# Performance work log

Hardware: AMD Instinct MI355X
Metric: run time of the kernel (lower is better)

The kernel has to match this reference:

```python
import jax, jax.numpy as jnp
import numpy as np

B, V, NX, R, D, H = 512, 2, 1024, 64, 512, 8
S, NC, HS = 4, 2, 64           # bc_state_dim, num_controls, state-branch hidden
FIN = S * HS + 128             # fusion input dim (state feats + control feats)


def _ln(x, g, b, eps=1e-5):
    mu = jnp.mean(x, axis=-1, keepdims=True)
    var = jnp.mean((x - mu) ** 2, axis=-1, keepdims=True)
    return (x - mu) * jax.lax.rsqrt(var + eps) * g + b


def setup_inputs() -> dict:
    key = jax.random.key(0)
    ks = iter(jax.random.split(key, 64))
    def rn(shape, s=0.02):
        return jax.random.normal(next(ks), shape, dtype=jnp.float32) * s
    inp = {}
    inp['a_n'] = jax.random.normal(next(ks), (B, V, R), dtype=jnp.float32)
    inp['BC_Ctrl'] = jax.random.normal(next(ks), (B, S + NC), dtype=jnp.float32)
    inp['Phi'] = rn((V, NX, R), 1.0 / np.sqrt(NX).astype(np.float32))
    # per-variable attention params (stacked on leading V axis)
    inp['Wq_w'] = rn((V, 1, D));   inp['Wq_b'] = rn((V, D))
    inp['Wk_w'] = rn((V, NX, D));  inp['Wk_b'] = rn((V, D))
    inp['Wv_w'] = rn((V, NX, D));  inp['Wv_b'] = rn((V, D))
    inp['attn_ow'] = rn((V, D, D)); inp['attn_ob'] = rn((V, D))
    inp['proj_w'] = rn((V, D, 1));  inp['proj_b'] = rn((V, 1))
    # ImprovedUpdateFFN (num_layers=3, hidden=d_model) + LayerNorm
    inp['ffn_w1'] = rn((V, R, D)); inp['ffn_b1'] = rn((V, D))
    inp['ffn_w2'] = rn((V, D, D)); inp['ffn_b2'] = rn((V, D))
    inp['ffn_w3'] = rn((V, D, R)); inp['ffn_b3'] = rn((V, R))
    inp['ffn_ln_g'] = jnp.ones((V, R), jnp.float32)
    inp['ffn_ln_b'] = jnp.zeros((V, R), jnp.float32)
    # a0_mapping: Linear -> ReLU -> LayerNorm
    inp['a0_w'] = rn((V, R, R)); inp['a0_b'] = rn((V, R))
    inp['a0_ln_g'] = jnp.ones((V, R), jnp.float32)
    inp['a0_ln_b'] = jnp.zeros((V, R), jnp.float32)
    inp['alpha'] = jnp.full((V,), 0.1, jnp.float32)
    # UniversalLifting params
    inp['sb_w'] = rn((S, 1, HS)); inp['sb_b'] = rn((S, HS))
    inp['cm_w1'] = rn((NC, 64));  inp['cm_b1'] = rn((64,))
    inp['cm_w2'] = rn((64, 128)); inp['cm_b2'] = rn((128,))
    inp['fu_w1'] = rn((FIN, 256)); inp['fu_b1'] = rn((256,))
    inp['fu_w2'] = rn((256, 512)); inp['fu_b2'] = rn((512,))
    inp['fu_w3'] = rn((512, 256)); inp['fu_b3'] = rn((256,))
    inp['fu_w4'] = rn((256, V * NX)); inp['fu_b4'] = rn((V * NX,))
    return inp


def reference(a_n, BC_Ctrl, Phi, Wq_w, Wq_b, Wk_w, Wk_b, Wv_w, Wv_b,
              attn_ow, attn_ob, proj_w, proj_b,
              ffn_w1, ffn_b1, ffn_w2, ffn_b2, ffn_w3, ffn_b3, ffn_ln_g, ffn_ln_b,
              a0_w, a0_b, a0_ln_g, a0_ln_b, alpha,
              sb_w, sb_b, cm_w1, cm_b1, cm_w2, cm_b2,
              fu_w1, fu_b1, fu_w2, fu_b2, fu_w3, fu_b3, fu_w4, fu_b4):
    gelu = jax.nn.gelu
    # ---- UniversalLifting: U_B [B, V, NX] ----
    bs = BC_Ctrl[:, :S]                                              # [B,S]
    sf = gelu(bs[:, :, None] * sb_w[None, :, 0, :] + sb_b[None])     # [B,S,HS]
    sf = sf.reshape(bs.shape[0], S * HS)
    cf = gelu(BC_Ctrl[:, S:] @ cm_w1 + cm_b1)
    cf = gelu(cf @ cm_w2 + cm_b2)
    f = jnp.concatenate([sf, cf], axis=-1)                           # [B,FIN]
    h = gelu(f @ fu_w1 + fu_b1)
    h = gelu(h @ fu_w2 + fu_b2)
    h = gelu(h @ fu_w3 + fu_b3)
    U_B = (h @ fu_w4 + fu_b4).reshape(-1, V, NX)
    # ---- a0 mapping: Linear -> ReLU -> LayerNorm ----
    a_map = jax.nn.relu(jnp.einsum('bvr,vrs->bvs', a_n, a0_w) + a0_b[None])
    a_map = _ln(a_map, a0_ln_g[None], a0_ln_b[None])                 # [B,V,R]
    # ---- ImprovedUpdateFFN residual update ----
    h1 = gelu(jnp.einsum('bvr,vrd->bvd', a_map, ffn_w1) + ffn_b1[None])
    h2 = gelu(jnp.einsum('bvd,vde->bve', h1, ffn_w2) + ffn_b2[None])
    o = jnp.einsum('bvd,vdr->bvr', h2, ffn_w3) + ffn_b3[None]
    ffn_update = _ln(o + a_map, ffn_ln_g[None], ffn_ln_b[None])      # [B,V,R]
    # ---- Q/K/V; K,V depend only on Phi (batch-independent) ----
    Q = a_map[:, :, :, None] * Wq_w[:, 0][None, :, None, :] + Wq_b[None, :, None, :]  # [B,V,R,D]
    K = jnp.einsum('vnr,vnd->vrd', Phi, Wk_w) + Wk_b[:, None, :]     # [V,R,D]
    Vm = jnp.einsum('vnr,vnd->vrd', Phi, Wv_w) + Wv_b[:, None, :]    # [V,R,D]
    hd = D // H
    Qh = Q.reshape(-1, V, R, H, hd)
    Kh = K.reshape(V, R, H, hd)
    Vh = Vm.reshape(V, R, H, hd)
    # softmax-free linear attention: z = Q (K^T V) per head
    KV = jnp.einsum('vrhk,vrhl->vhkl', Kh, Vh)                        # [V,H,hd,hd]
    z = jnp.einsum('bvrhk,vhkl->bvrhl', Qh, KV).reshape(-1, V, R, D)
    z = jnp.einsum('bvrd,vde->bvre', z, attn_ow) + attn_ob[None, :, None, :]
    z = z / jnp.sqrt(jnp.float32(D))
    a_update = jnp.einsum('bvrd,vdo->bvro', z, proj_w)[..., 0] + proj_b[:, 0][None, :, None]
    a_next = a_map + a_update + alpha[None, :, None] * ffn_update     # [B,V,R]
    U_hat = jnp.einsum('vnr,bvr->bvn', Phi, a_next) + U_B             # [B,V,NX]
    return U_hat
```

## Files before the change

### kernel.cpp

```cpp
#include <hip/hip_runtime.h>
#include <hip/hip_bf16.h>
#include <math.h>


typedef unsigned short ushort_t;
using short8 = __attribute__((ext_vector_type(8))) short;
using f32x4  = __attribute__((ext_vector_type(4))) float;

__device__ __forceinline__ float gelu_f(float x) {
    float x3 = x*x*x;
    return 0.5f*x*(1.0f + tanhf(0.7978845608028654f*(x + 0.044715f*x3)));
}

__device__ __forceinline__ float wave_sum(float x) {
    #pragma unroll
    for (int m = 32; m >= 1; m >>= 1) x += __shfl_xor(x, m, 64);
    return x;
}

__device__ __forceinline__ ushort_t f2bf(float x) {
    unsigned u = __float_as_uint(x);
    unsigned r = (u + 0x7FFFu + ((u >> 16) & 1u)) >> 16;
    return (ushort_t)r;
}
__device__ __forceinline__ float bf2f(ushort_t h) {
    return __uint_as_float(((unsigned)h) << 16);
}

struct Ptrs {
    const float *a_n, *BC, *Wq_w, *Wq_b, *Wk_b, *Wv_b, *attn_ow, *attn_ob,
                *proj_w, *proj_b, *ffn_w3, *ffn_b3, *ffn_ln_g, *ffn_ln_b,
                *a0_w, *a0_b, *a0_ln_g, *a0_ln_b, *alpha,
                *sb_w, *sb_b, *cm_w1, *cm_b1, *cm_w2, *cm_b2,
                *fu_b1, *fu_b2, *fu_b3, *fu_b4, *ffn_b1, *ffn_b2;
    float *Kws, *Vws, *KV, *parts, *UB, *out;
    ushort_t *amap_bf, *anext_bf, *h1_bf, *h2_bf, *fbuf_bf, *hA_bf, *hB_bf, *hC_bf;
    ushort_t *w_fu1t, *w_fu2t, *w_fu3t, *w_fu4t, *w_ffn1t, *w_ffn2t,
             *Phi_bf, *Wk_t, *Wv_t, *Phi_t;
};

struct CvtDesc { const float* src; ushort_t* dst; int K, N, flat; };
struct CvtArgs { CvtDesc d[15]; int cum[16]; };

__device__ void cvt_dev(char* smem, int tile, const CvtDesc& d)
{
    const int t = threadIdx.x;
    if (d.flat) {
        const long base = (long)tile*4096 + t*16;
        const float4* s = (const float4*)(d.src + base);
        ushort4* o = (ushort4*)(d.dst + base);
        #pragma unroll
        for (int i = 0; i < 4; ++i) {
            float4 v = s[i];
            ushort4 w; w.x=f2bf(v.x); w.y=f2bf(v.y); w.z=f2bf(v.z); w.w=f2bf(v.w);
            o[i] = w;
        }
    } else {
        float* tl = (float*)smem;
        const int ntn = d.N >> 5;
        const int kt = tile / ntn, nt = tile % ntn;
        const int r = t >> 3, c0 = (t & 7) * 4;
        float4 v = *(const float4*)(d.src + (long)(kt*32 + r)*d.N + nt*32 + c0);
        tl[r*33 + c0] = v.x; tl[r*33 + c0+1] = v.y;
        tl[r*33 + c0+2] = v.z; tl[r*33 + c0+3] = v.w;
        __syncthreads();
        ushort4 w;
        w.x = f2bf(tl[(c0+0)*33 + r]); w.y = f2bf(tl[(c0+1)*33 + r]);
        w.z = f2bf(tl[(c0+2)*33 + r]); w.w = f2bf(tl[(c0+3)*33 + r]);
        *(ushort4*)(d.dst + (long)(nt*32 + r)*d.K + kt*32 + c0) = w;
    }
}

__device__ void bgemm_dev(char* smem_,
    const ushort_t* __restrict__ A, const ushort_t* __restrict__ B,
    const float* __restrict__ bias, const float* __restrict__ Add,
    void* __restrict__ Cv, int m0, int n0, int K, int ldc, int ldadd,
    int EPI, bool OUTBF)
{
    ushort_t* lds = (ushort_t*)smem_;
    const int tid = threadIdx.x;
    const int w = tid >> 6, l = tid & 63;
    const int ml = l & 15, kg = l >> 4;
    const int srow = tid >> 2, sslot = tid & 3;
    const ushort_t* Ag = A + (long)(m0 + srow)*K + sslot*8;
    const ushort_t* Bg = B + (long)(n0 + srow)*K + sslot*8;
    auto L = [&](int buf, int ab, int row, int col) {
        return lds + (((buf*2 + ab)*64 + row)*40 + col);
    };
    f32x4 acc[4] = {};
    const int nt = K >> 5;
    int4 ra = *(const int4*)Ag;
    int4 rb = *(const int4*)Bg;
    *(int4*)L(0,0,srow,sslot*8) = ra;
    *(int4*)L(0,1,srow,sslot*8) = rb;
    __syncthreads();
    for (int t = 0; t < nt; ++t) {
        const int cur = t & 1;
        if (t + 1 < nt) {
            ra = *(const int4*)(Ag + (t+1)*32);
            rb = *(const int4*)(Bg + (t+1)*32);
        }
        short8 af = *(const short8*)L(cur,0,w*16 + ml,kg*8);
        #pragma unroll
        for (int f = 0; f < 4; ++f) {
            short8 bfr = *(const short8*)L(cur,1,f*16 + ml,kg*8);
            acc[f] = __builtin_amdgcn_mfma_f32_16x16x32_bf16(af, bfr, acc[f], 0, 0, 0);
        }
        if (t + 1 < nt) {
            *(int4*)L(cur^1,0,srow,sslot*8) = ra;
            *(int4*)L(cur^1,1,srow,sslot*8) = rb;
            __syncthreads();
        }
    }
    float* Cf = (float*)Cv; ushort_t* Cb = (ushort_t*)Cv;
    const int mr = m0 + w*16 + kg*4;
    const int nc = n0 + ml;
    #pragma unroll
    for (int f = 0; f < 4; ++f) {
        const int n = nc + f*16;
        const float bs = (EPI != 2) ? bias[n] : 0.0f;
        #pragma unroll
        for (int r = 0; r < 4; ++r) {
            float x = acc[f][r] + bs;
            if (EPI == 1) x = gelu_f(x);
            if (EPI == 2) x = acc[f][r] + Add[(long)(mr + r)*ldadd + n];
            if (OUTBF) Cb[(long)(mr + r)*ldc + n] = f2bf(x);
            else       Cf[(long)(mr + r)*ldc + n] = x;
        }
    }
}

__device__ void control_dev(char* smem, int b, const Ptrs& p)
{
    float* bc  = (float*)smem;
    float* cf1 = bc + 8;
    const int tid = threadIdx.x;
    if (tid < 6) bc[tid] = p.BC[b*6 + tid];
    __syncthreads();
    {
        int s = tid >> 6;
        p.fbuf_bf[(long)b*384 + tid] = f2bf(gelu_f(bc[s]*p.sb_w[tid] + p.sb_b[tid]));
    }
    if (tid < 64) {
        cf1[tid] = gelu_f(bc[4]*p.cm_w1[tid] + bc[5]*p.cm_w1[64+tid] + p.cm_b1[tid]);
    }
    __syncthreads();
    if (tid < 128) {
        float acc = p.cm_b2[tid];
        #pragma unroll 8
        for (int i = 0; i < 64; ++i) acc = fmaf(cf1[i], p.cm_w2[i*128 + tid], acc);
        p.fbuf_bf[(long)b*384 + 256 + tid] = f2bf(gelu_f(acc));
    }
}

__device__ void a_map_dev(char* smem, int bx, int v, const Ptrs& p)
{
    float* arow = (float*)smem;
    const int w = threadIdx.x >> 6, lane = threadIdx.x & 63;
    const int b = bx*4 + w;
    arow[w*64 + lane] = p.a_n[((long)b*2 + v)*64 + lane];
    __syncthreads();
    float acc = p.a0_b[v*64 + lane];
    #pragma unroll 8
    for (int rp = 0; rp < 64; ++rp)
        acc = fmaf(arow[w*64 + rp], p.a0_w[((long)v*64 + rp)*64 + lane], acc);
    float x = fmaxf(acc, 0.0f);
    float mu = wave_sum(x) * (1.0f/64.0f);
    float d = x - mu;
    float var = wave_sum(d*d) * (1.0f/64.0f);
    float y = d * rsqrtf(var + 1e-5f) * p.a0_ln_g[v*64 + lane] + p.a0_ln_b[v*64 + lane];
    p.amap_bf[((long)v*512 + b)*64 + lane] = f2bf(y);
}

__device__ void kv_outer_dev(char* smem, int z, const Ptrs& p)
{
    const int v = z >> 3, h = z & 7;
    float* Ks = (float*)smem;
    float* Vs = Ks + 4096;
    const int tid = threadIdx.x;
    for (int idx = tid; idx < 4096; idx += 256) {
        int r = idx >> 6, c = idx & 63;
        long off = ((long)v*64 + r)*512 + h*64 + c;
        Ks[idx] = p.Kws[off];
        Vs[idx] = p.Vws[off];
    }
    __syncthreads();
    const int tx = tid & 15, ty = tid >> 4;
    float acc[4][4] = {};
    #pragma unroll 4
    for (int r = 0; r < 64; ++r) {
        float a[4], bb[4];
        #pragma unroll
        for (int i = 0; i < 4; ++i) a[i] = Ks[r*64 + ty*4+i];
        #pragma unroll
        for (int j = 0; j < 4; ++j) bb[j] = Vs[r*64 + tx*4+j];
        #pragma unroll
        for (int i = 0; i < 4; ++i)
            #pragma unroll
            for (int j = 0; j < 4; ++j)
                acc[i][j] = fmaf(a[i], bb[j], acc[i][j]);
    }
    #pragma unroll
    for (int i = 0; i < 4; ++i)
        #pragma unroll
        for (int j = 0; j < 4; ++j)
            p.KV[(((long)v*8 + h)*64 + ty*4+i)*64 + tx*4+j] = acc[i][j];
}

__device__ void attn_parts_dev(char* smem, int v, int ec, const Ptrs& p)
{
    float* Pv  = (float*)smem;
    float* Qv  = Pv + 512;
    float* red = Qv + 512;
    const int tid = threadIdx.x;
    for (int dp = tid; dp < 512; dp += 256) {
        int h = dp >> 6, l = dp & 63;
        const float* kvp = p.KV + ((long)(v*8 + h)*64)*64 + l;
        const float* wq = p.Wq_w + v*512 + h*64;
        const float* wb = p.Wq_b + v*512 + h*64;
        float pp = 0.f, q = 0.f;
        #pragma unroll 8
        for (int k = 0; k < 64; ++k) {
            float kv = kvp[(long)k*64];
            pp = fmaf(wq[k], kv, pp);
            q  = fmaf(wb[k], kv, q);
        }
        Pv[dp] = pp; Qv[dp] = q;
    }
    __syncthreads();
    const int e = ec*64 + (tid & 63);
    const int qd = tid >> 6;
    float pw = 0.f, qw = 0.f;
    const float* owp = p.attn_ow + (long)v*512*512 + e;
    #pragma unroll 8
    for (int d = qd*128; d < qd*128 + 128; ++d) {
        float wv = owp[(long)d*512];
        pw = fmaf(Pv[d], wv, pw);
        qw = fmaf(Qv[d], wv, qw);
    }
    red[tid] = pw; red[256 + tid] = qw;
    __syncthreads();
    if (tid < 64) {
        float PW = red[tid] + red[tid+64] + red[tid+128] + red[tid+192];
        float QW = red[256+tid] + red[256+tid+64] + red[256+tid+128] + red[256+tid+192];
        QW += p.attn_ob[v*512 + ec*64 + tid];
        float pj = p.proj_w[v*512 + ec*64 + tid];
        float pc1 = wave_sum(PW*pj);
        float pc0 = wave_sum(QW*pj);
        if (tid == 0) {
            p.parts[v*8 + ec]      = pc1;
            p.parts[16 + v*8 + ec] = pc0;
        }
    }
}

__device__ void ofuse_dev(char* smem, int bx, int v, const Ptrs& p)
{
    float* hrow = (float*)smem;
    const int w = threadIdx.x >> 6, lane = threadIdx.x & 63;
    const int b = bx*4 + w;
    const ushort_t* h2p = p.h2_bf + ((long)v*512 + b)*512;
    #pragma unroll
    for (int i = 0; i < 8; ++i) hrow[w*512 + lane + i*64] = bf2f(h2p[lane + i*64]);
    __syncthreads();
    float acc = p.ffn_b3[v*64 + lane];
    const float* w3p = p.ffn_w3 + (long)v*512*64 + lane;
    #pragma unroll 8
    for (int d = 0; d < 512; ++d)
        acc = fmaf(hrow[w*512 + d], w3p[(long)d*64], acc);
    const float am = bf2f(p.amap_bf[((long)v*512 + b)*64 + lane]);
    float t = acc + am;
    float mu = wave_sum(t) * (1.0f/64.0f);
    float dd = t - mu;
    float var = wave_sum(dd*dd) * (1.0f/64.0f);
    float u = dd * rsqrtf(var + 1e-5f) * p.ffn_ln_g[v*64+lane] + p.ffn_ln_b[v*64+lane];
    float s1 = 0.f, s0 = 0.f;
    #pragma unroll
    for (int c = 0; c < 8; ++c) { s1 += p.parts[v*8 + c]; s0 += p.parts[16 + v*8 + c]; }
    const float inv = 0.044194173824159216f;
    const float c1 = s1*inv, c0 = s0*inv + p.proj_b[v];
    p.anext_bf[((long)v*512 + b)*64 + lane] = f2bf(am*(1.0f + c1) + c0 + p.alpha[v]*u);
}

__global__ __launch_bounds__(256) void stage0_k(Ptrs p, CvtArgs ca, int ncvt)
{
    extern __shared__ char smem[];
    const int bx = blockIdx.x;
    if (bx < ncvt) {
        int e = 0;
        while (bx >= ca.cum[e+1]) ++e;
        cvt_dev(smem, bx - ca.cum[e], ca.d[e]);
    } else if (bx < ncvt + 512) {
        control_dev(smem, bx - ncvt, p);
    } else {
        int i = bx - ncvt - 512;
        a_map_dev(smem, i & 127, i >> 7, p);
    }
}

__global__ __launch_bounds__(256) void stage1_k(Ptrs p)
{
    extern __shared__ char smem[];
    const int bx = blockIdx.x;
    if (bx < 32) {
        int by = bx >> 2, bxx = bx & 3;
        bgemm_dev(smem, p.fbuf_bf, p.w_fu1t, p.fu_b1, nullptr, p.hA_bf,
                  by*64, bxx*64, 384, 256, 0, 1, true);
    } else if (bx < 160) {
        int i = bx - 32; int v = i >> 6; i &= 63; int by = i >> 3, bxx = i & 7;
        bgemm_dev(smem, p.amap_bf + (long)v*32768, p.w_ffn1t + (long)v*32768,
                  p.ffn_b1 + v*512, nullptr, (void*)(p.h1_bf + (long)v*262144),
                  by*64, bxx*64, 64, 512, 0, 1, true);
    } else {
        int i = bx - 160; int which = i >> 4; int v = (i >> 3) & 1; int bxx = i & 7;
        const ushort_t* Wt = which ? p.Wv_t : p.Wk_t;
        const float* Wb = which ? p.Wv_b : p.Wk_b;
        float* C = which ? p.Vws : p.Kws;
        bgemm_dev(smem, p.Phi_t + (long)v*65536, Wt + (long)v*524288,
                  Wb + v*512, nullptr, (void*)(C + (long)v*32768),
                  0, bxx*64, 1024, 512, 0, 0, false);
    }
}

__global__ __launch_bounds__(256) void stage2_k(Ptrs p)
{
    extern __shared__ char smem[];
    const int bx = blockIdx.x;
    if (bx < 64) {
        int by = bx >> 3, bxx = bx & 7;
        bgemm_dev(smem, p.hA_bf, p.w_fu2t, p.fu_b2, nullptr, p.hB_bf,
                  by*64, bxx*64, 256, 512, 0, 1, true);
    } else if (bx < 192) {
        int i = bx - 64; int v = i >> 6; i &= 63; int by = i >> 3, bxx = i & 7;
        bgemm_dev(smem, p.h1_bf + (long)v*262144, p.w_ffn2t + (long)v*262144,
                  p.ffn_b2 + v*512, nullptr, (void*)(p.h2_bf + (long)v*262144),
                  by*64, bxx*64, 512, 512, 0, 1, true);
    } else {
        kv_outer_dev(smem, bx - 192, p);
    }
}

__global__ __launch_bounds__(256) void stage3_k(Ptrs p)
{
    extern __shared__ char smem[];
    const int bx = blockIdx.x;
    if (bx < 32) {
        int by = bx >> 2, bxx = bx & 3;
        bgemm_dev(smem, p.hB_bf, p.w_fu3t, p.fu_b3, nullptr, p.hC_bf,
                  by*64, bxx*64, 512, 256, 0, 1, true);
    } else {
        int i = bx - 32;
        attn_parts_dev(smem, i & 1, i >> 1, p);
    }
}

__global__ __launch_bounds__(256) void stage4_k(Ptrs p)
{
    extern __shared__ char smem[];
    const int bx = blockIdx.x;
    if (bx < 256) {
        int by = bx >> 5, bxx = bx & 31;
        bgemm_dev(smem, p.hC_bf, p.w_fu4t, p.fu_b4, nullptr, p.UB,
                  by*64, bxx*64, 256, 2048, 0, 0, false);
    } else {
        int i = bx - 256;
        ofuse_dev(smem, i & 127, i >> 7, p);
    }
}

__global__ __launch_bounds__(256) void stage5_k(Ptrs p)
{
    extern __shared__ char smem[];
    const int bx = blockIdx.x;
    int v = bx >> 7; int rem = bx & 127; int by = rem >> 4, bxx = rem & 15;
    bgemm_dev(smem, p.anext_bf + (long)v*32768, p.Phi_bf + (long)v*65536,
              nullptr, p.UB + v*1024, (void*)(p.out + v*1024),
              by*64, bxx*64, 64, 2048, 2048, 2, false);
}

extern "C" void kernel_launch(void* const* d_in, const int* in_sizes, int n_in,
                              void* d_out, int out_size, void* d_ws, size_t ws_size,
                              hipStream_t stream)
{
    const float* a_n      = (const float*)d_in[0];
    const float* BC       = (const float*)d_in[1];
    const float* Phi      = (const float*)d_in[2];
    const float* Wq_w     = (const float*)d_in[3];
    const float* Wq_b     = (const float*)d_in[4];
    const float* Wk_w     = (const float*)d_in[5];
    const float* Wk_b     = (const float*)d_in[6];
    const float* Wv_w     = (const float*)d_in[7];
    const float* Wv_b     = (const float*)d_in[8];
    const float* attn_ow  = (const float*)d_in[9];
    const float* attn_ob  = (const float*)d_in[10];
    const float* proj_w   = (const float*)d_in[11];
    const float* proj_b   = (const float*)d_in[12];
    const float* ffn_w1   = (const float*)d_in[13];
    const float* ffn_b1   = (const float*)d_in[14];
    const float* ffn_w2   = (const float*)d_in[15];
    const float* ffn_b2   = (const float*)d_in[16];
    const float* ffn_w3   = (const float*)d_in[17];
    const float* ffn_b3   = (const float*)d_in[18];
    const float* ffn_ln_g = (const float*)d_in[19];
    const float* ffn_ln_b = (const float*)d_in[20];
    const float* a0_w     = (const float*)d_in[21];
    const float* a0_b     = (const float*)d_in[22];
    const float* a0_ln_g  = (const float*)d_in[23];
    const float* a0_ln_b  = (const float*)d_in[24];
    const float* alpha    = (const float*)d_in[25];
    const float* sb_w     = (const float*)d_in[26];
    const float* sb_b     = (const float*)d_in[27];
    const float* cm_w1    = (const float*)d_in[28];
    const float* cm_b1    = (const float*)d_in[29];
    const float* cm_w2    = (const float*)d_in[30];
    const float* cm_b2    = (const float*)d_in[31];
    const float* fu_w1    = (const float*)d_in[32];
    const float* fu_b1    = (const float*)d_in[33];
    const float* fu_w2    = (const float*)d_in[34];
    const float* fu_b2    = (const float*)d_in[35];
    const float* fu_w3    = (const float*)d_in[36];
    const float* fu_b3    = (const float*)d_in[37];
    const float* fu_w4    = (const float*)d_in[38];
    const float* fu_b4    = (const float*)d_in[39];

    float* ws = (float*)d_ws;
    Ptrs p;
    p.a_n = a_n; p.BC = BC; p.Wq_w = Wq_w; p.Wq_b = Wq_b; p.Wk_b = Wk_b; p.Wv_b = Wv_b;
    p.attn_ow = attn_ow; p.attn_ob = attn_ob; p.proj_w = proj_w; p.proj_b = proj_b;
    p.ffn_w3 = ffn_w3; p.ffn_b3 = ffn_b3; p.ffn_ln_g = ffn_ln_g; p.ffn_ln_b = ffn_ln_b;
    p.a0_w = a0_w; p.a0_b = a0_b; p.a0_ln_g = a0_ln_g; p.a0_ln_b = a0_ln_b;
    p.alpha = alpha; p.sb_w = sb_w; p.sb_b = sb_b;
    p.cm_w1 = cm_w1; p.cm_b1 = cm_b1; p.cm_w2 = cm_w2; p.cm_b2 = cm_b2;
    p.fu_b1 = fu_b1; p.fu_b2 = fu_b2; p.fu_b3 = fu_b3; p.fu_b4 = fu_b4;
    p.ffn_b1 = ffn_b1; p.ffn_b2 = ffn_b2;

    p.Kws      = ws;
    p.Vws      = ws + 65536;
    p.KV       = ws + 131072;
    p.parts    = ws + 196608;
    p.amap_bf  = (ushort_t*)(ws + 196736);
    p.anext_bf = (ushort_t*)(ws + 229504);
    p.h1_bf    = (ushort_t*)(ws + 262272);
    p.h2_bf    = (ushort_t*)(ws + 524416);
    p.fbuf_bf  = (ushort_t*)(ws + 786560);
    p.hA_bf    = (ushort_t*)(ws + 884864);
    p.hB_bf    = (ushort_t*)(ws + 950400);
    p.hC_bf    = (ushort_t*)(ws + 1081472);
    p.w_fu1t   = (ushort_t*)(ws + 1147008);
    p.w_fu2t   = (ushort_t*)(ws + 1196160);
    p.w_fu3t   = (ushort_t*)(ws + 1261696);
    p.w_fu4t   = (ushort_t*)(ws + 1327232);
    p.w_ffn1t  = (ushort_t*)(ws + 1589376);
    p.w_ffn2t  = (ushort_t*)(ws + 1622144);
    p.Phi_bf   = (ushort_t*)(ws + 1884288);
    p.UB       = ws + 1949824;
    p.Wk_t     = (ushort_t*)p.UB;
    p.Wv_t     = ((ushort_t*)p.UB) + 1048576;
    p.Phi_t    = (ushort_t*)(ws + 2998400);
    p.out      = (float*)d_out;

    CvtArgs ca;
    auto set = [&](int i, const float* s, ushort_t* dst, int K, int N, int flat) {
        ca.d[i].src = s; ca.d[i].dst = dst; ca.d[i].K = K; ca.d[i].N = N; ca.d[i].flat = flat;
    };
    set(0,  fu_w1,           p.w_fu1t,           384, 256,  0);
    set(1,  fu_w2,           p.w_fu2t,           256, 512,  0);
    set(2,  fu_w3,           p.w_fu3t,           512, 256,  0);
    set(3,  fu_w4,           p.w_fu4t,           256, 2048, 0);
    set(4,  ffn_w1,          p.w_ffn1t,          64,  512,  0);
    set(5,  ffn_w1 + 32768,  p.w_ffn1t + 32768,  64,  512,  0);
    set(6,  ffn_w2,          p.w_ffn2t,          512, 512,  0);
    set(7,  ffn_w2 + 262144, p.w_ffn2t + 262144, 512, 512,  0);
    set(8,  Phi,             p.Phi_bf,           131072, 0, 1);
    set(9,  Phi,             p.Phi_t,            1024, 64,  0);
    set(10, Phi + 65536,     p.Phi_t + 65536,    1024, 64,  0);
    set(11, Wk_w,            p.Wk_t,             1024, 512, 0);
    set(12, Wk_w + 524288,   p.Wk_t + 524288,    1024, 512, 0);
    set(13, Wv_w,            p.Wv_t,             1024, 512, 0);
    set(14, Wv_w + 524288,   p.Wv_t + 524288,    1024, 512, 0);
    const int tl[15] = {96,128,128,512,32,32,256,256,32,64,64,512,512,512,512};
    ca.cum[0] = 0;
    for (int i = 0; i < 15; ++i) ca.cum[i+1] = ca.cum[i] + tl[i];
    const int ncvt = ca.cum[15];

    stage0_k<<<ncvt + 768, 256, 4352,  stream>>>(p, ca, ncvt);
    stage1_k<<<192,        256, 20480, stream>>>(p);
    stage2_k<<<208,        256, 32768, stream>>>(p);
    stage3_k<<<48,         256, 20480, stream>>>(p);
    stage4_k<<<512,        256, 20480, stream>>>(p);
    stage5_k<<<256,        256, 20480, stream>>>(p);
}
```

Baseline: 77.58 us.

## Fold attention into per-variable scalars and merge final GEMMs into one K=384 GEMM

The batch-independent K/V/out-projection chain is collapsed algebraically. Matrix-vector products (attn_ow·proj_w, Wk·Wq, Wv·opj, then contractions with Phi) reduce the whole attention branch to two scalars per variable. This removes the large Phi×Wk/Wv GEMMs, the KV outer products and their bf16 conversions. The fusion-net output GEMM and the Phi reconstruction GEMM are combined into a single GEMM over a concatenated K dimension, with a precomputed bias row, which cuts one launch and the UB round trip. The cost is a different summation order, so numerical results may shift slightly.

```diff
diff --git a/kernel.cpp b/kernel.cpp
--- a/kernel.cpp
+++ b/kernel.cpp
@@ -28,33 +28,41 @@
 }
 
 struct Ptrs {
-    const float *a_n, *BC, *Wq_w, *Wq_b, *Wk_b, *Wv_b, *attn_ow, *attn_ob,
-                *proj_w, *proj_b, *ffn_w3, *ffn_b3, *ffn_ln_g, *ffn_ln_b,
+    const float *a_n, *BC, *Phi, *Wq_w, *Wq_b, *Wk_w, *Wk_b, *Wv_w, *Wv_b,
+                *attn_ow, *attn_ob, *proj_w, *proj_b,
+                *ffn_w3, *ffn_b3, *ffn_ln_g, *ffn_ln_b,
                 *a0_w, *a0_b, *a0_ln_g, *a0_ln_b, *alpha,
                 *sb_w, *sb_b, *cm_w1, *cm_b1, *cm_w2, *cm_b2,
                 *fu_b1, *fu_b2, *fu_b3, *fu_b4, *ffn_b1, *ffn_b2;
-    float *Kws, *Vws, *KV, *parts, *UB, *out;
-    ushort_t *amap_bf, *anext_bf, *h1_bf, *h2_bf, *fbuf_bf, *hA_bf, *hB_bf, *hC_bf;
-    ushort_t *w_fu1t, *w_fu2t, *w_fu3t, *w_fu4t, *w_ffn1t, *w_ffn2t,
-             *Phi_bf, *Wk_t, *Wv_t, *Phi_t;
+    float *opj, *u0, *u1, *u2, *pkq, *pqq, *parts, *phirs, *bias2, *out;
+    ushort_t *amap_bf, *h1_bf, *h2_bf, *fbuf_bf, *hA_bf, *hB_bf;
+    ushort_t *w_fu1t, *w_fu2t, *w_fu3t, *w_ffn1t, *w_ffn2t, *Abig, *Bbig;
 };
 
-struct CvtDesc { const float* src; ushort_t* dst; int K, N, flat; };
-struct CvtArgs { CvtDesc d[15]; int cum[16]; };
-
-__device__ void cvt_dev(char* smem, int tile, const CvtDesc& d)
+struct CvtDesc { const float* src; ushort_t* dst; int K, N, mode, ldd, coff; };
+struct CvtArgs { CvtDesc d[10]; int cum[11]; };
+
+__device__ void cvt_dev(char* smem, int tile, const CvtDesc& d, const Ptrs& p)
 {
     const int t = threadIdx.x;
-    if (d.flat) {
-        const long base = (long)tile*4096 + t*16;
-        const float4* s = (const float4*)(d.src + base);
-        ushort4* o = (ushort4*)(d.dst + base);
+    if (d.mode == 2) {
+        const int row = t >> 2, q = t & 3;
+        const float* s = d.src + (long)(tile*64 + row)*64 + q*16;
+        ushort_t* dst  = d.dst + (long)(tile*64 + row)*384 + d.coff + q*16;
+        ushort_t* dz   = d.dst + (long)(tile*64 + row)*384 + (64 - d.coff) + q*16;
+        float sum = 0.f;
         #pragma unroll
         for (int i = 0; i < 4; ++i) {
-            float4 v = s[i];
-            ushort4 w; w.x=f2bf(v.x); w.y=f2bf(v.y); w.z=f2bf(v.z); w.w=f2bf(v.w);
-            o[i] = w;
-        }
+            float4 x = *(const float4*)(s + i*4);
+            ushort4 w; w.x=f2bf(x.x); w.y=f2bf(x.y); w.z=f2bf(x.z); w.w=f2bf(x.w);
+            *(ushort4*)(dst + i*4) = w;
+            ushort4 z; z.x=0; z.y=0; z.z=0; z.w=0;
+            *(ushort4*)(dz + i*4) = z;
+            sum += x.x + x.y + x.z + x.w;
+        }
+        sum += __shfl_xor(sum, 1, 64);
+        sum += __shfl_xor(sum, 2, 64);
+        if (q == 0) p.phirs[d.K + tile*64 + row] = sum;
     } else {
         float* tl = (float*)smem;
         const int ntn = d.N >> 5;
@@ -67,14 +75,14 @@
         ushort4 w;
         w.x = f2bf(tl[(c0+0)*33 + r]); w.y = f2bf(tl[(c0+1)*33 + r]);
         w.z = f2bf(tl[(c0+2)*33 + r]); w.w = f2bf(tl[(c0+3)*33 + r]);
-        *(ushort4*)(d.dst + (long)(nt*32 + r)*d.K + kt*32 + c0) = w;
+        *(ushort4*)(d.dst + (long)(nt*32 + r)*d.ldd + d.coff + kt*32 + c0) = w;
     }
 }
 
 __device__ void bgemm_dev(char* smem_,
     const ushort_t* __restrict__ A, const ushort_t* __restrict__ B,
-    const float* __restrict__ bias, const float* __restrict__ Add,
-    void* __restrict__ Cv, int m0, int n0, int K, int ldc, int ldadd,
+    const float* __restrict__ bias,
+    void* __restrict__ Cv, int m0, int n0, int K, int ldc,
     int EPI, bool OUTBF)
 {
     ushort_t* lds = (ushort_t*)smem_;
@@ -118,12 +126,11 @@
     #pragma unroll
     for (int f = 0; f < 4; ++f) {
         const int n = nc + f*16;
-        const float bs = (EPI != 2) ? bias[n] : 0.0f;
+        const float bs = bias[n];
         #pragma unroll
         for (int r = 0; r < 4; ++r) {
             float x = acc[f][r] + bs;
             if (EPI == 1) x = gelu_f(x);
-            if (EPI == 2) x = acc[f][r] + Add[(long)(mr + r)*ldadd + n];
             if (OUTBF) Cb[(long)(mr + r)*ldc + n] = f2bf(x);
             else       Cf[(long)(mr + r)*ldc + n] = x;
         }
@@ -172,85 +179,143 @@
     p.amap_bf[((long)v*512 + b)*64 + lane] = f2bf(y);
 }
 
-__device__ void kv_outer_dev(char* smem, int z, const Ptrs& p)
-{
-    const int v = z >> 3, h = z & 7;
-    float* Ks = (float*)smem;
-    float* Vs = Ks + 4096;
-    const int tid = threadIdx.x;
-    for (int idx = tid; idx < 4096; idx += 256) {
-        int r = idx >> 6, c = idx & 63;
-        long off = ((long)v*64 + r)*512 + h*64 + c;
-        Ks[idx] = p.Kws[off];
-        Vs[idx] = p.Vws[off];
-    }
+__device__ void opj_dev(int oi, const Ptrs& p)
+{
+    const int tid = threadIdx.x;
+    const int v = oi >> 3, dc = oi & 7;
+    const int d = dc*64 + (tid >> 2);
+    const int e0 = (tid & 3)*128;
+    const float* row = p.attn_ow + ((long)v*512 + d)*512 + e0;
+    const float* pj  = p.proj_w + v*512 + e0;
+    float s = 0.f;
+    #pragma unroll 8
+    for (int j = 0; j < 128; ++j) s = fmaf(row[j], pj[j], s);
+    s += __shfl_xor(s, 1, 64);
+    s += __shfl_xor(s, 2, 64);
+    if ((tid & 3) == 0) p.opj[v*512 + d] = s;
+}
+
+__device__ void u01_dev(int i, const Ptrs& p)
+{
+    const int tid = threadIdx.x;
+    const int w = tid >> 6, lane = tid & 63;
+    const int v = i >> 4, c = i & 15;
+    const float* wq = p.Wq_w + v*512;
+    const float* wb = p.Wq_b + v*512;
+    for (int pass = 0; pass < 16; ++pass) {
+        const int n = c*64 + pass*4 + w;
+        const float* row = p.Wk_w + ((long)v*1024 + n)*512 + lane*8;
+        float4 a = *(const float4*)row, b = *(const float4*)(row + 4);
+        float s0 = 0.f, s1 = 0.f;
+        #pragma unroll
+        for (int j = 0; j < 8; ++j) {
+            float x = (j < 4) ? ((const float*)&a)[j] : ((const float*)&b)[j-4];
+            s0 = fmaf(x, wq[lane*8 + j], s0);
+            s1 = fmaf(x, wb[lane*8 + j], s1);
+        }
+        s0 += __shfl_xor(s0,1,64); s0 += __shfl_xor(s0,2,64); s0 += __shfl_xor(s0,4,64);
+        s1 += __shfl_xor(s1,1,64); s1 += __shfl_xor(s1,2,64); s1 += __shfl_xor(s1,4,64);
+        if ((lane & 7) == 0) {
+            const int h = lane >> 3;
+            p.u0[((long)v*1024 + n)*8 + h] = s0;
+            p.u1[((long)v*1024 + n)*8 + h] = s1;
+        }
+    }
+}
+
+__device__ void u2_dev(int i, const Ptrs& p)
+{
+    const int tid = threadIdx.x;
+    const int w = tid >> 6, lane = tid & 63;
+    const int v = i >> 4, c = i & 15;
+    const float* oj = p.opj + v*512;
+    for (int pass = 0; pass < 16; ++pass) {
+        const int n = c*64 + pass*4 + w;
+        const float* row = p.Wv_w + ((long)v*1024 + n)*512 + lane*8;
+        float4 a = *(const float4*)row, b = *(const float4*)(row + 4);
+        float s0 = 0.f;
+        #pragma unroll
+        for (int j = 0; j < 8; ++j) {
+            float x = (j < 4) ? ((const float*)&a)[j] : ((const float*)&b)[j-4];
+            s0 = fmaf(x, oj[lane*8 + j], s0);
+        }
+        s0 += __shfl_xor(s0,1,64); s0 += __shfl_xor(s0,2,64); s0 += __shfl_xor(s0,4,64);
+        if ((lane & 7) == 0) p.u2[((long)v*1024 + n)*8 + (lane >> 3)] = s0;
+    }
+}
+
+__device__ void kqqq_dev(int i, const Ptrs& p)
+{
+    const int tid = threadIdx.x;
+    const int v = i >> 3, c = i & 7;
+    const int r = tid & 63, hp = tid >> 6;
+    const int h0 = hp*2, h1 = h0 + 1;
+    float k0=0.f,k1=0.f,q0=0.f,q1=0.f;
+    const float* Pb = p.Phi + ((long)v*1024 + c*128)*64 + r;
+    const float* U0 = p.u0 + ((long)v*1024 + c*128)*8;
+    const float* U1 = p.u1 + ((long)v*1024 + c*128)*8;
+    #pragma unroll 4
+    for (int n = 0; n < 128; ++n) {
+        float phi = Pb[(long)n*64];
+        k0 = fmaf(phi, U0[n*8+h0], k0); k1 = fmaf(phi, U0[n*8+h1], k1);
+        q0 = fmaf(phi, U1[n*8+h0], q0); q1 = fmaf(phi, U1[n*8+h1], q1);
+    }
+    const long o = (((long)v*8 + c)*64 + r)*8;
+    p.pkq[o+h0] = k0; p.pkq[o+h1] = k1;
+    p.pqq[o+h0] = q0; p.pqq[o+h1] = q1;
+}
+
+__device__ void consts2_dev(char* smem, int v, const Ptrs& p)
+{
+    const int tid = threadIdx.x;
+    const int r = tid & 63, hp = tid >> 6;
+    const int h0 = hp*2, h1 = h0 + 1;
+    float vo0 = 0.f, vo1 = 0.f;
+    const float* Pb = p.Phi + ((long)v*1024)*64 + r;
+    const float* U2 = p.u2 + ((long)v*1024)*8;
+    #pragma unroll 4
+    for (int n = 0; n < 1024; ++n) {
+        float phi = Pb[(long)n*64];
+        vo0 = fmaf(phi, U2[n*8+h0], vo0);
+        vo1 = fmaf(phi, U2[n*8+h1], vo1);
+    }
+    float k0=0.f,k1=0.f,q0=0.f,q1=0.f;
+    #pragma unroll
+    for (int c = 0; c < 8; ++c) {
+        const long o = (((long)v*8 + c)*64 + r)*8;
+        k0 += p.pkq[o+h0]; k1 += p.pkq[o+h1];
+        q0 += p.pqq[o+h0]; q1 += p.pqq[o+h1];
+    }
+    float bk0=0.f,bk1=0.f,bq0=0.f,bq1=0.f,bv0=0.f,bv1=0.f;
+    #pragma unroll 8
+    for (int j = 0; j < 64; ++j) {
+        float b0 = p.Wk_b[v*512 + h0*64 + j], b1 = p.Wk_b[v*512 + h1*64 + j];
+        bk0 = fmaf(b0, p.Wq_w[v*512 + h0*64 + j], bk0);
+        bk1 = fmaf(b1, p.Wq_w[v*512 + h1*64 + j], bk1);
+        bq0 = fmaf(b0, p.Wq_b[v*512 + h0*64 + j], bq0);
+        bq1 = fmaf(b1, p.Wq_b[v*512 + h1*64 + j], bq1);
+        float c0v = p.Wv_b[v*512 + h0*64 + j], c1v = p.Wv_b[v*512 + h1*64 + j];
+        bv0 = fmaf(c0v, p.opj[v*512 + h0*64 + j], bv0);
+        bv1 = fmaf(c1v, p.opj[v*512 + h1*64 + j], bv1);
+    }
+    vo0 += bv0; vo1 += bv1;
+    k0 += bk0; k1 += bk1; q0 += bq0; q1 += bq1;
+    float s1 = k0*vo0 + k1*vo1;
+    float s0 = q0*vo0 + q1*vo1;
+    float sA = p.attn_ob[v*512 + tid]*p.proj_w[v*512 + tid]
+             + p.attn_ob[v*512 + 256 + tid]*p.proj_w[v*512 + 256 + tid];
+    s1 = wave_sum(s1); s0 = wave_sum(s0); sA = wave_sum(sA);
+    float* red = (float*)smem;
+    const int w = tid >> 6, l = tid & 63;
+    if (l == 0) { red[w] = s1; red[4+w] = s0; red[8+w] = sA; }
     __syncthreads();
-    const int tx = tid & 15, ty = tid >> 4;
-    float acc[4][4] = {};
-    #pragma unroll 4
-    for (int r = 0; r < 64; ++r) {
-        float a[4], bb[4];
-        #pragma unroll
-        for (int i = 0; i < 4; ++i) a[i] = Ks[r*64 + ty*4+i];
-        #pragma unroll
-        for (int j = 0; j < 4; ++j) bb[j] = Vs[r*64 + tx*4+j];
-        #pragma unroll
-        for (int i = 0; i < 4; ++i)
-            #pragma unroll
-            for (int j = 0; j < 4; ++j)
-                acc[i][j] = fmaf(a[i], bb[j], acc[i][j]);
-    }
-    #pragma unroll
-    for (int i = 0; i < 4; ++i)
-        #pragma unroll
-        for (int j = 0; j < 4; ++j)
-            p.KV[(((long)v*8 + h)*64 + ty*4+i)*64 + tx*4+j] = acc[i][j];
-}
-
-__device__ void attn_parts_dev(char* smem, int v, int ec, const Ptrs& p)
-{
-    float* Pv  = (float*)smem;
-    float* Qv  = Pv + 512;
-    float* red = Qv + 512;
-    const int tid = threadIdx.x;
-    for (int dp = tid; dp < 512; dp += 256) {
-        int h = dp >> 6, l = dp & 63;
-        const float* kvp = p.KV + ((long)(v*8 + h)*64)*64 + l;
-        const float* wq = p.Wq_w + v*512 + h*64;
-        const float* wb = p.Wq_b + v*512 + h*64;
-        float pp = 0.f, q = 0.f;
-        #pragma unroll 8
-        for (int k = 0; k < 64; ++k) {
-            float kv = kvp[(long)k*64];
-            pp = fmaf(wq[k], kv, pp);
-            q  = fmaf(wb[k], kv, q);
-        }
-        Pv[dp] = pp; Qv[dp] = q;
-    }
-    __syncthreads();
-    const int e = ec*64 + (tid & 63);
-    const int qd = tid >> 6;
-    float pw = 0.f, qw = 0.f;
-    const float* owp = p.attn_ow + (long)v*512*512 + e;
-    #pragma unroll 8
-    for (int d = qd*128; d < qd*128 + 128; ++d) {
-        float wv = owp[(long)d*512];
-        pw = fmaf(Pv[d], wv, pw);
-        qw = fmaf(Qv[d], wv, qw);
-    }
-    red[tid] = pw; red[256 + tid] = qw;
-    __syncthreads();
-    if (tid < 64) {
-        float PW = red[tid] + red[tid+64] + red[tid+128] + red[tid+192];
-        float QW = red[256+tid] + red[256+tid+64] + red[256+tid+128] + red[256+tid+192];
-        QW += p.attn_ob[v*512 + ec*64 + tid];
-        float pj = p.proj_w[v*512 + ec*64 + tid];
-        float pc1 = wave_sum(PW*pj);
-        float pc0 = wave_sum(QW*pj);
-        if (tid == 0) {
-            p.parts[v*8 + ec]      = pc1;
-            p.parts[16 + v*8 + ec] = pc0;
-        }
+    if (tid == 0) {
+        float S1 = red[0]+red[1]+red[2]+red[3];
+        float S0 = red[4]+red[5]+red[6]+red[7];
+        float SA = red[8]+red[9]+red[10]+red[11];
+        const float inv = 0.044194173824159216f;
+        p.parts[v]     = S1*inv;
+        p.parts[2 + v] = (S0 + SA)*inv + p.proj_b[v];
     }
 }
 
@@ -274,12 +339,18 @@
     float dd = t - mu;
     float var = wave_sum(dd*dd) * (1.0f/64.0f);
     float u = dd * rsqrtf(var + 1e-5f) * p.ffn_ln_g[v*64+lane] + p.ffn_ln_b[v*64+lane];
-    float s1 = 0.f, s0 = 0.f;
+    const float c1 = p.parts[v];
+    p.Abig[(long)b*384 + v*64 + lane] = f2bf(am*(1.0f + c1) + p.alpha[v]*u);
+}
+
+__device__ void bias2_dev(const Ptrs& p)
+{
     #pragma unroll
-    for (int c = 0; c < 8; ++c) { s1 += p.parts[v*8 + c]; s0 += p.parts[16 + v*8 + c]; }
-    const float inv = 0.044194173824159216f;
-    const float c1 = s1*inv, c0 = s0*inv + p.proj_b[v];
-    p.anext_bf[((long)v*512 + b)*64 + lane] = f2bf(am*(1.0f + c1) + c0 + p.alpha[v]*u);
+    for (int k = 0; k < 8; ++k) {
+        const int n2 = k*256 + threadIdx.x;
+        const int v = n2 >> 10;
+        p.bias2[n2] = p.fu_b4[n2] + p.parts[2+v]*p.phirs[n2];
+    }
 }
 
 __global__ __launch_bounds__(256) void stage0_k(Ptrs p, CvtArgs ca, int ncvt)
@@ -289,12 +360,16 @@
     if (bx < ncvt) {
         int e = 0;
         while (bx >= ca.cum[e+1]) ++e;
-        cvt_dev(smem, bx - ca.cum[e], ca.d[e]);
+        cvt_dev(smem, bx - ca.cum[e], ca.d[e], p);
     } else if (bx < ncvt + 512) {
         control_dev(smem, bx - ncvt, p);
-    } else {
+    } else if (bx < ncvt + 768) {
         int i = bx - ncvt - 512;
         a_map_dev(smem, i & 127, i >> 7, p);
+    } else if (bx < ncvt + 784) {
+        opj_dev(bx - ncvt - 768, p);
+    } else {
+        u01_dev(bx - ncvt - 784, p);
     }
 }
 
@@ -303,22 +378,17 @@
     extern __shared__ char smem[];
     const int bx = blockIdx.x;
     if (bx < 32) {
-        int by = bx >> 2, bxx = bx & 3;
-        bgemm_dev(smem, p.fbuf_bf, p.w_fu1t, p.fu_b1, nullptr, p.hA_bf,
-                  by*64, bxx*64, 384, 256, 0, 1, true);
+        bgemm_dev(smem, p.fbuf_bf, p.w_fu1t, p.fu_b1, p.hA_bf,
+                  (bx>>2)*64, (bx&3)*64, 384, 256, 1, true);
     } else if (bx < 160) {
-        int i = bx - 32; int v = i >> 6; i &= 63; int by = i >> 3, bxx = i & 7;
+        int i = bx - 32; int v = i >> 6; i &= 63;
         bgemm_dev(smem, p.amap_bf + (long)v*32768, p.w_ffn1t + (long)v*32768,
-                  p.ffn_b1 + v*512, nullptr, (void*)(p.h1_bf + (long)v*262144),
-                  by*64, bxx*64, 64, 512, 0, 1, true);
+                  p.ffn_b1 + v*512, (void*)(p.h1_bf + (long)v*262144),
+                  (i>>3)*64, (i&7)*64, 64, 512, 1, true);
+    } else if (bx < 192) {
+        u2_dev(bx - 160, p);
     } else {
-        int i = bx - 160; int which = i >> 4; int v = (i >> 3) & 1; int bxx = i & 7;
-        const ushort_t* Wt = which ? p.Wv_t : p.Wk_t;
-        const float* Wb = which ? p.Wv_b : p.Wk_b;
-        float* C = which ? p.Vws : p.Kws;
-        bgemm_dev(smem, p.Phi_t + (long)v*65536, Wt + (long)v*524288,
-                  Wb + v*512, nullptr, (void*)(C + (long)v*32768),
-                  0, bxx*64, 1024, 512, 0, 0, false);
+        kqqq_dev(bx - 192, p);
     }
 }
 
@@ -327,16 +397,15 @@
     extern __shared__ char smem[];
     const int bx = blockIdx.x;
     if (bx < 64) {
-        int by = bx >> 3, bxx = bx & 7;
-        bgemm_dev(smem, p.hA_bf, p.w_fu2t, p.fu_b2, nullptr, p.hB_bf,
-                  by*64, bxx*64, 256, 512, 0, 1, true);
+        bgemm_dev(smem, p.hA_bf, p.w_fu2t, p.fu_b2, p.hB_bf,
+                  (bx>>3)*64, (bx&7)*64, 256, 512, 1, true);
     } else if (bx < 192) {
-        int i = bx - 64; int v = i >> 6; i &= 63; int by = i >> 3, bxx = i & 7;
+        int i = bx - 64; int v = i >> 6; i &= 63;
         bgemm_dev(smem, p.h1_bf + (long)v*262144, p.w_ffn2t + (long)v*262144,
-                  p.ffn_b2 + v*512, nullptr, (void*)(p.h2_bf + (long)v*262144),
-                  by*64, bxx*64, 512, 512, 0, 1, true);
+                  p.ffn_b2 + v*512, (void*)(p.h2_bf + (long)v*262144),
+                  (i>>3)*64, (i&7)*64, 512, 512, 1, true);
     } else {
-        kv_outer_dev(smem, bx - 192, p);
+        consts2_dev(smem, bx - 192, p);
     }
 }
 
@@ -345,12 +414,13 @@
     extern __shared__ char smem[];
     const int bx = blockIdx.x;
     if (bx < 32) {
-        int by = bx >> 2, bxx = bx & 3;
-        bgemm_dev(smem, p.hB_bf, p.w_fu3t, p.fu_b3, nullptr, p.hC_bf,
-                  by*64, bxx*64, 512, 256, 0, 1, true);
+        bgemm_dev(smem, p.hB_bf, p.w_fu3t, p.fu_b3, (void*)(p.Abig + 128),
+                  (bx>>2)*64, (bx&3)*64, 512, 384, 1, true);
+    } else if (bx < 288) {
+        int i = bx - 32;
+        ofuse_dev(smem, i & 127, i >> 7, p);
     } else {
-        int i = bx - 32;
-        attn_parts_dev(smem, i & 1, i >> 1, p);
+        bias2_dev(p);
     }
 }
 
@@ -358,24 +428,8 @@
 {
     extern __shared__ char smem[];
     const int bx = blockIdx.x;
-    if (bx < 256) {
-        int by = bx >> 5, bxx = bx & 31;
-        bgemm_dev(smem, p.hC_bf, p.w_fu4t, p.fu_b4, nullptr, p.UB,
-                  by*64, bxx*64, 256, 2048, 0, 0, false);
-    } else {
-        int i = bx - 256;
-        ofuse_dev(smem, i & 127, i >> 7, p);
-    }
-}
-
-__global__ __launch_bounds__(256) void stage5_k(Ptrs p)
-{
-    extern __shared__ char smem[];
-    const int bx = blockIdx.x;
-    int v = bx >> 7; int rem = bx & 127; int by = rem >> 4, bxx = rem & 15;
-    bgemm_dev(smem, p.anext_bf + (long)v*32768, p.Phi_bf + (long)v*65536,
-              nullptr, p.UB + v*1024, (void*)(p.out + v*1024),
-              by*64, bxx*64, 64, 2048, 2048, 2, false);
+    bgemm_dev(smem, p.Abig, p.Bbig, p.bias2, (void*)p.out,
+              (bx>>5)*64, (bx&31)*64, 384, 2048, 0, false);
 }
 
 extern "C" void kernel_launch(void* const* d_in, const int* in_sizes, int n_in,
@@ -425,7 +479,8 @@
 
     float* ws = (float*)d_ws;
     Ptrs p;
-    p.a_n = a_n; p.BC = BC; p.Wq_w = Wq_w; p.Wq_b = Wq_b; p.Wk_b = Wk_b; p.Wv_b = Wv_b;
+    p.a_n = a_n; p.BC = BC; p.Phi = Phi; p.Wq_w = Wq_w; p.Wq_b = Wq_b;
+    p.Wk_w = Wk_w; p.Wk_b = Wk_b; p.Wv_w = Wv_w; p.Wv_b = Wv_b;
     p.attn_ow = attn_ow; p.attn_ob = attn_ob; p.proj_w = proj_w; p.proj_b = proj_b;
     p.ffn_w3 = ffn_w3; p.ffn_b3 = ffn_b3; p.ffn_ln_g = ffn_ln_g; p.ffn_ln_b = ffn_ln_b;
     p.a0_w = a0_w; p.a0_b = a0_b; p.a0_ln_g = a0_ln_g; p.a0_ln_b = a0_ln_b;
@@ -434,59 +489,54 @@
     p.fu_b1 = fu_b1; p.fu_b2 = fu_b2; p.fu_b3 = fu_b3; p.fu_b4 = fu_b4;
     p.ffn_b1 = ffn_b1; p.ffn_b2 = ffn_b2;
 
-    p.Kws      = ws;
-    p.Vws      = ws + 65536;
-    p.KV       = ws + 131072;
-    p.parts    = ws + 196608;
-    p.amap_bf  = (ushort_t*)(ws + 196736);
-    p.anext_bf = (ushort_t*)(ws + 229504);
-    p.h1_bf    = (ushort_t*)(ws + 262272);
-    p.h2_bf    = (ushort_t*)(ws + 524416);
-    p.fbuf_bf  = (ushort_t*)(ws + 786560);
-    p.hA_bf    = (ushort_t*)(ws + 884864);
-    p.hB_bf    = (ushort_t*)(ws + 950400);
-    p.hC_bf    = (ushort_t*)(ws + 1081472);
-    p.w_fu1t   = (ushort_t*)(ws + 1147008);
-    p.w_fu2t   = (ushort_t*)(ws + 1196160);
-    p.w_fu3t   = (ushort_t*)(ws + 1261696);
-    p.w_fu4t   = (ushort_t*)(ws + 1327232);
-    p.w_ffn1t  = (ushort_t*)(ws + 1589376);
-    p.w_ffn2t  = (ushort_t*)(ws + 1622144);
-    p.Phi_bf   = (ushort_t*)(ws + 1884288);
-    p.UB       = ws + 1949824;
-    p.Wk_t     = (ushort_t*)p.UB;
-    p.Wv_t     = ((ushort_t*)p.UB) + 1048576;
-    p.Phi_t    = (ushort_t*)(ws + 2998400);
-    p.out      = (float*)d_out;
+    p.opj     = ws;
+    p.u0      = ws + 1024;
+    p.u1      = ws + 17408;
+    p.u2      = ws + 33792;
+    p.pkq     = ws + 50176;
+    p.pqq     = ws + 58368;
+    p.parts   = ws + 66560;
+    p.phirs   = ws + 66576;
+    p.bias2   = ws + 68624;
+    p.amap_bf = (ushort_t*)(ws + 70672);
+    p.h1_bf   = (ushort_t*)(ws + 103440);
+    p.h2_bf   = (ushort_t*)(ws + 365584);
+    p.fbuf_bf = (ushort_t*)(ws + 627728);
+    p.hA_bf   = (ushort_t*)(ws + 726032);
+    p.hB_bf   = (ushort_t*)(ws + 791568);
+    p.w_fu1t  = (ushort_t*)(ws + 922640);
+    p.w_fu2t  = (ushort_t*)(ws + 971792);
+    p.w_fu3t  = (ushort_t*)(ws + 1037328);
+    p.w_ffn1t = (ushort_t*)(ws + 1102864);
+    p.w_ffn2t = (ushort_t*)(ws + 1135632);
+    p.Abig    = (ushort_t*)(ws + 1397776);
+    p.Bbig    = (ushort_t*)(ws + 1496080);
+    p.out     = (float*)d_out;
 
     CvtArgs ca;
-    auto set = [&](int i, const float* s, ushort_t* dst, int K, int N, int flat) {
-        ca.d[i].src = s; ca.d[i].dst = dst; ca.d[i].K = K; ca.d[i].N = N; ca.d[i].flat = flat;
+    auto set = [&](int i, const float* s, ushort_t* dst, int K, int N,
+                   int mode, int ldd, int coff) {
+        ca.d[i].src = s; ca.d[i].dst = dst; ca.d[i].K = K; ca.d[i].N = N;
+        ca.d[i].mode = mode; ca.d[i].ldd = ldd; ca.d[i].coff = coff;
     };
-    set(0,  fu_w1,           p.w_fu1t,           384, 256,  0);
-    set(1,  fu_w2,           p.w_fu2t,           256, 512,  0);
-    set(2,  fu_w3,           p.w_fu3t,           512, 256,  0);
-    set(3,  fu_w4,           p.w_fu4t,           256, 2048, 0);
-    set(4,  ffn_w1,          p.w_ffn1t,          64,  512,  0);
-    set(5,  ffn_w1 + 32768,  p.w_ffn1t + 32768,  64,  512,  0);
-    set(6,  ffn_w2,          p.w_ffn2t,          512, 512,  0);
-    set(7,  ffn_w2 + 262144, p.w_ffn2t + 262144, 512, 512,  0);
-    set(8,  Phi,             p.Phi_bf,           131072, 0, 1);
-    set(9,  Phi,             p.Phi_t,            1024, 64,  0);
-    set(10, Phi + 65536,     p.Phi_t + 65536,    1024, 64,  0);
-    set(11, Wk_w,            p.Wk_t,             1024, 512, 0);
-    set(12, Wk_w + 524288,   p.Wk_t + 524288,    1024, 512, 0);
-    set(13, Wv_w,            p.Wv_t,             1024, 512, 0);
-    set(14, Wv_w + 524288,   p.Wv_t + 524288,    1024, 512, 0);
-    const int tl[15] = {96,128,128,512,32,32,256,256,32,64,64,512,512,512,512};
+    set(0, fu_w1,            p.w_fu1t,           384, 256,  0, 384, 0);
+    set(1, fu_w2,            p.w_fu2t,           256, 512,  0, 256, 0);
+    set(2, fu_w3,            p.w_fu3t,           512, 256,  0, 512, 0);
+    set(3, fu_w4,            p.Bbig,             256, 2048, 0, 384, 128);
+    set(4, ffn_w1,           p.w_ffn1t,          64,  512,  0, 64,  0);
+    set(5, ffn_w1 + 32768,   p.w_ffn1t + 32768,  64,  512,  0, 64,  0);
+    set(6, ffn_w2,           p.w_ffn2t,          512, 512,  0, 512, 0);
+    set(7, ffn_w2 + 262144,  p.w_ffn2t + 262144, 512, 512,  0, 512, 0);
+    set(8, Phi,              p.Bbig,             0,    0,   2, 384, 0);
+    set(9, Phi + 65536,      p.Bbig + (long)1024*384, 1024, 0, 2, 384, 64);
+    const int tl[10] = {96,128,128,512,32,32,256,256,16,16};
     ca.cum[0] = 0;
-    for (int i = 0; i < 15; ++i) ca.cum[i+1] = ca.cum[i] + tl[i];
-    const int ncvt = ca.cum[15];
-
-    stage0_k<<<ncvt + 768, 256, 4352,  stream>>>(p, ca, ncvt);
-    stage1_k<<<192,        256, 20480, stream>>>(p);
-    stage2_k<<<208,        256, 32768, stream>>>(p);
-    stage3_k<<<48,         256, 20480, stream>>>(p);
-    stage4_k<<<512,        256, 20480, stream>>>(p);
-    stage5_k<<<256,        256, 20480, stream>>>(p);
-}
+    for (int i = 0; i < 10; ++i) ca.cum[i+1] = ca.cum[i] + tl[i];
+    const int ncvt = ca.cum[10];
+
+    stage0_k<<<ncvt + 816, 256, 4352,  stream>>>(p, ca, ncvt);
+    stage1_k<<<208,        256, 20480, stream>>>(p);
+    stage2_k<<<194,        256, 20480, stream>>>(p);
+    stage3_k<<<289,        256, 20480, stream>>>(p);
+    stage4_k<<<256,        256, 20480, stream>>>(p);
+}
```

New measurement: 144.1 us. 1.86x slower.
